# Optimization experiments

Measured on AMD Instinct MI355X. Metric: run time of the kernel, lower is better.

The kernel has to match this reference:

```python
import jax, jax.numpy as jnp
import numpy as np

D = 256      # model_dim
H = 8        # num_heads
S = 256      # tokens per channel
CH = [4, 2, 6, 4]  # multiplex_channels_per_sample


def _make_padding(ch, s):
    # Build gather indices / mask mapping packed tokens [T] -> padded [B, Lmax]
    B = len(ch)
    lens = [c * s for c in ch]
    T = sum(lens)
    Lmax = max(lens)
    pad_idx = np.zeros((B, Lmax), dtype=np.int32)
    pad_mask = np.zeros((B, Lmax), dtype=bool)
    off = 0
    for b, L in enumerate(lens):
        pad_idx[b, :L] = np.arange(off, off + L, dtype=np.int32)
        pad_mask[b, :L] = True
        off += L
    return jnp.asarray(pad_idx), jnp.asarray(pad_mask)


def setup_inputs() -> dict:
    key = jax.random.key(0)
    ks = jax.random.split(key, 16)
    C = sum(CH)
    x_query = jax.random.normal(ks[0], (C, S, D), jnp.float32)
    x_keyval = jax.random.normal(ks[1], (C, S, D), jnp.float32)
    pos = jax.random.normal(ks[2], (C, S, D), jnp.float32)
    pad_idx, pad_mask = _make_padding(CH, S)
    sc = 1.0 / np.sqrt(D)
    Wq = jax.random.normal(ks[3], (D, D), jnp.float32) * sc
    Wk = jax.random.normal(ks[4], (D, D), jnp.float32) * sc
    Wv = jax.random.normal(ks[5], (D, D), jnp.float32) * sc
    Wo = jax.random.normal(ks[6], (D, D), jnp.float32) * sc
    bq = jax.random.normal(ks[7], (D,), jnp.float32) * 0.02
    bk = jax.random.normal(ks[8], (D,), jnp.float32) * 0.02
    bv = jax.random.normal(ks[9], (D,), jnp.float32) * 0.02
    bo = jax.random.normal(ks[10], (D,), jnp.float32) * 0.02
    return {"x_query": x_query, "x_keyval": x_keyval, "pos": pos,
            "pad_idx": pad_idx, "pad_mask": pad_mask,
            "Wq": Wq, "bq": bq, "Wk": Wk, "bk": bk,
            "Wv": Wv, "bv": bv, "Wo": Wo, "bo": bo}


def reference(x_query, x_keyval, pos, pad_idx, pad_mask,
              Wq, bq, Wk, bk, Wv, bv, Wo, bo):
    C, s, d = x_query.shape
    T = C * s
    dh = d // H
    # MHA with positional embedding: pos is added to query and key inputs
    # (query_pos = key_pos = pos in the original forward), value is raw.
    q_in = (x_query + pos).reshape(T, d)
    k_in = (x_keyval + pos).reshape(T, d)
    v_in = x_keyval.reshape(T, d)
    q = q_in @ Wq + bq
    k = k_in @ Wk + bk
    v = v_in @ Wv + bv
    # Pad packed ragged tokens into [B, Lmax, D] per cu_seq_len segments
    B, Lmax = pad_idx.shape
    qp = q[pad_idx].reshape(B, Lmax, H, dh)
    kp = k[pad_idx].reshape(B, Lmax, H, dh)
    vp = v[pad_idx].reshape(B, Lmax, H, dh)
    scores = jnp.einsum('bqhd,bkhd->bhqk', qp, kp) / jnp.sqrt(jnp.asarray(dh, q.dtype))
    neg = jnp.asarray(jnp.finfo(scores.dtype).min, scores.dtype)
    scores = jnp.where(pad_mask[:, None, None, :], scores, neg)
    attn = jax.nn.softmax(scores, axis=-1)
    out = jnp.einsum('bhqk,bkhd->bqhd', attn, vp).reshape(B, Lmax, d)
    out = out * pad_mask[..., None]
    # Scatter padded outputs back to packed layout [T, D]
    flat = jnp.zeros((T, d), out.dtype).at[pad_idx.reshape(-1)].add(out.reshape(-1, d))
    flat = flat @ Wo + bo
    return flat.reshape(C, s, d)
```

## Files before the change

kernel.cpp:

```cpp
#include <hip/hip_runtime.h>
#include <math.h>

#define Dm 256
#define Tt 4096

typedef short  s16x8 __attribute__((ext_vector_type(8)));
typedef float  f32x4 __attribute__((ext_vector_type(4)));

__device__ __forceinline__ ushort f2bf(float x) {
    union { float f; unsigned u; } v; v.f = x;
    unsigned r = v.u + 0x7fffu + ((v.u >> 16) & 1u);
    return (ushort)(r >> 16);
}

__device__ __forceinline__ int ppos(int row, int key) {
    return row * 64 + (key & 7) + ((((key >> 3) ^ (row >> 1)) & 7) << 3);
}

__global__ __launch_bounds__(256)
void convert_x(const float* __restrict__ xq, const float* __restrict__ xkv,
               const float* __restrict__ pos,
               ushort* __restrict__ A0, ushort* __restrict__ A1, ushort* __restrict__ A2)
{
    const int t = threadIdx.x;
    const int m = blockIdx.y;
    const float* xin = (m == 0) ? xq : xkv;
    ushort* out = (m == 0) ? A0 : (m == 1) ? A1 : A2;
    const int token = blockIdx.x * 32 + (t >> 3);
    const int c0 = (t & 7) * 32;
    const float* p = &xin[token * Dm + c0];
    const float* pp = &pos[token * Dm + c0];
    #pragma unroll
    for (int i = 0; i < 4; ++i) {
        float4 fa = *(const float4*)&p[i * 8];
        float4 fb = *(const float4*)&p[i * 8 + 4];
        if (m < 2) {
            float4 pa = *(const float4*)&pp[i * 8], pb = *(const float4*)&pp[i * 8 + 4];
            fa.x += pa.x; fa.y += pa.y; fa.z += pa.z; fa.w += pa.w;
            fb.x += pb.x; fb.y += pb.y; fb.z += pb.z; fb.w += pb.w;
        }
        s16x8 v8;
        v8[0] = (short)f2bf(fa.x); v8[1] = (short)f2bf(fa.y);
        v8[2] = (short)f2bf(fa.z); v8[3] = (short)f2bf(fa.w);
        v8[4] = (short)f2bf(fb.x); v8[5] = (short)f2bf(fb.y);
        v8[6] = (short)f2bf(fb.z); v8[7] = (short)f2bf(fb.w);
        *(s16x8*)&out[token * Dm + c0 + i * 8] = v8;
    }
}

__global__ __launch_bounds__(256)
void prep_w(const float* __restrict__ Wq, const float* __restrict__ Wk,
            const float* __restrict__ Wv, const float* __restrict__ Wo,
            ushort* __restrict__ Wt)
{
    __shared__ float T[64][65];
    const int tid = threadIdx.x;
    const int m = blockIdx.y;
    const int i = blockIdx.x >> 2, j = blockIdx.x & 3;
    const float* W = (m == 0) ? Wq : (m == 1) ? Wk : (m == 2) ? Wv : Wo;

    #pragma unroll
    for (int s = 0; s < 4; ++s) {
        int idx = s * 256 + tid;
        int r = idx >> 4, c4 = (idx & 15) << 2;
        float4 f = *(const float4*)&W[(i * 64 + r) * Dm + j * 64 + c4];
        T[c4 + 0][r] = f.x; T[c4 + 1][r] = f.y;
        T[c4 + 2][r] = f.z; T[c4 + 3][r] = f.w;
    }
    __syncthreads();
    #pragma unroll
    for (int s = 0; s < 2; ++s) {
        int idx = s * 256 + tid;
        int cr = idx >> 3, k8 = (idx & 7) << 3;
        s16x8 v8;
        #pragma unroll
        for (int jj = 0; jj < 8; ++jj) v8[jj] = (short)f2bf(T[cr][k8 + jj]);
        *(s16x8*)&Wt[m * 65536 + (j * 64 + cr) * Dm + i * 64 + k8] = v8;
    }
}

__global__ __launch_bounds__(256)
void proj_gemm(const ushort* __restrict__ A0, const ushort* __restrict__ A1,
               const ushort* __restrict__ A2, const ushort* __restrict__ Wt,
               const float* __restrict__ bq, const float* __restrict__ bk,
               const float* __restrict__ bv,
               ushort* __restrict__ qo, ushort* __restrict__ ko, ushort* __restrict__ vo)
{
    __shared__ __align__(16) ushort A_s[64 * 64];
    __shared__ __align__(16) ushort B_s[64 * 64];
    const int tid = threadIdx.x;
    const int lane = tid & 63, g = lane >> 4, myrow = lane & 15, w = tid >> 6;
    const int t0 = blockIdx.x * 64;
    const int c0 = blockIdx.y * 64;
    const int m  = blockIdx.z;
    const ushort* Ab = (m == 0) ? A0 : (m == 1) ? A1 : A2;
    const ushort* WT = Wt + m * 65536;
    const float* bias = (m == 0) ? bq : (m == 1) ? bk : bv;
    ushort* out = (m == 0) ? qo : (m == 1) ? ko : vo;

    f32x4 acc[4] = {};
    for (int ks = 0; ks < 4; ++ks) {
        const int k0 = ks * 64;
        #pragma unroll
        for (int s = 0; s < 2; ++s) {
            int idx = s * 256 + tid;
            int r = idx >> 3, c = idx & 7;
            *(s16x8*)&A_s[r * 64 + ((c ^ (r & 7)) << 3)] =
                *(const s16x8*)&Ab[(t0 + r) * Dm + k0 + c * 8];
            *(s16x8*)&B_s[r * 64 + ((c ^ (r & 7)) << 3)] =
                *(const s16x8*)&WT[(c0 + r) * Dm + k0 + c * 8];
        }
        __syncthreads();
        const int arow = w * 16 + myrow;
        #pragma unroll
        for (int kk = 0; kk < 2; ++kk) {
            s16x8 a = *(s16x8*)&A_s[arow * 64 + (((g + 4 * kk) ^ (arow & 7)) << 3)];
            #pragma unroll
            for (int ct = 0; ct < 4; ++ct) {
                int brow = ct * 16 + myrow;
                s16x8 b = *(s16x8*)&B_s[brow * 64 + (((g + 4 * kk) ^ (brow & 7)) << 3)];
                acc[ct] = __builtin_amdgcn_mfma_f32_16x16x32_bf16(a, b, acc[ct], 0, 0, 0);
            }
        }
        __syncthreads();
    }
    const float qsc = 0.17677669529663687f;
    #pragma unroll
    for (int ct = 0; ct < 4; ++ct) {
        int col = c0 + ct * 16 + myrow;
        float bval = bias[col];
        #pragma unroll
        for (int r = 0; r < 4; ++r) {
            int tok = t0 + w * 16 + 4 * g + r;
            float vv = acc[ct][r] + bval;
            if (m == 0) vv *= qsc;
            out[tok * Dm + col] = f2bf(vv);
        }
    }
}

__global__ __launch_bounds__(256)
void transp_v(const ushort* __restrict__ v, ushort* __restrict__ vT)
{
    __shared__ __align__(16) ushort T_s[64 * 72];
    const int tid = threadIdx.x;
    const int t0 = blockIdx.x * 64;
    const int c0 = blockIdx.y * 64;
    #pragma unroll
    for (int s = 0; s < 2; ++s) {
        int idx = s * 256 + tid;
        int row = idx >> 3, c8 = (idx & 7) << 3;
        s16x8 d = *(const s16x8*)&v[(t0 + row) * Dm + c0 + c8];
        #pragma unroll
        for (int j = 0; j < 8; ++j) {
            int c = c8 + j;
            T_s[c * 72 + (row ^ ((c & 7) << 3))] = (ushort)d[j];
        }
    }
    __syncthreads();
    #pragma unroll
    for (int s = 0; s < 2; ++s) {
        int idx = s * 256 + tid;
        int c = idx >> 3, k8 = (idx & 7) << 3;
        s16x8 d = *(const s16x8*)&T_s[c * 72 + (k8 ^ ((c & 7) << 3))];
        *(s16x8*)&vT[(c0 + c) * Tt + t0 + k8] = d;
    }
}

__global__ __launch_bounds__(256)
void attn3(const ushort* __restrict__ q, const ushort* __restrict__ kb,
           const ushort* __restrict__ vT, ushort* __restrict__ o)
{
    __shared__ __align__(16) ushort P_s[4][16 * 64];
    __shared__ float cmb[96 * 36];
    const int tid = threadIdx.x;
    const int lane = tid & 63, g = lane >> 4, myrow = lane & 15, w = tid >> 6;
    const int h = blockIdx.x & 7, qt = blockIdx.x >> 3;

    int off, L;
    if (qt < 32)      { off = 0;    L = 1024; }
    else if (qt < 48) { off = 1024; L = 512;  }
    else if (qt < 96) { off = 1536; L = 1536; }
    else              { off = 3072; L = 1024; }
    const int qrow0 = qt * 32;
    const int Lw = L >> 2;
    const int kbeg = off + w * Lw;
    const int ntk = Lw >> 6;

    s16x8 qf[2];
    qf[0] = *(const s16x8*)&q[(qrow0 + myrow) * Dm + h * 32 + g * 8];
    qf[1] = *(const s16x8*)&q[(qrow0 + 16 + myrow) * Dm + h * 32 + g * 8];

    f32x4 aO[2][2] = {};
    float mr[2][4], lr[2][4];
    #pragma unroll
    for (int s = 0; s < 2; ++s)
        #pragma unroll
        for (int r = 0; r < 4; ++r) { mr[s][r] = -INFINITY; lr[s][r] = 0.f; }

    for (int t = 0; t < ntk; ++t) {
        const int kt0 = kbeg + t * 64;
        s16x8 kf[4];
        #pragma unroll
        for (int kt = 0; kt < 4; ++kt)
            kf[kt] = *(const s16x8*)&kb[(kt0 + kt * 16 + myrow) * Dm + h * 32 + g * 8];
        s16x8 vfa[2], vfb[2];
        #pragma unroll
        for (int kk = 0; kk < 2; ++kk) {
            vfa[kk] = *(const s16x8*)&vT[(h * 32 + myrow) * Tt + kt0 + kk * 32 + g * 8];
            vfb[kk] = *(const s16x8*)&vT[(h * 32 + 16 + myrow) * Tt + kt0 + kk * 32 + g * 8];
        }

        #pragma unroll
        for (int s = 0; s < 2; ++s) {
            const f32x4 zero = {};
            f32x4 s4[4];
            #pragma unroll
            for (int kt = 0; kt < 4; ++kt)
                s4[kt] = __builtin_amdgcn_mfma_f32_16x16x32_bf16(qf[s], kf[kt], zero, 0, 0, 0);

            float mt[4], sc[4], ps[4];
            #pragma unroll
            for (int r = 0; r < 4; ++r) {
                float a = fmaxf(fmaxf(s4[0][r], s4[1][r]), fmaxf(s4[2][r], s4[3][r]));
                a = fmaxf(a, __shfl_xor(a, 1));
                a = fmaxf(a, __shfl_xor(a, 2));
                a = fmaxf(a, __shfl_xor(a, 4));
                a = fmaxf(a, __shfl_xor(a, 8));
                mt[r] = a;
            }
            #pragma unroll
            for (int r = 0; r < 4; ++r) {
                float mn = fmaxf(mr[s][r], mt[r]);
                sc[r] = __expf(mr[s][r] - mn);
                mr[s][r] = mn;
                ps[r] = 0.f;
            }
            asm volatile("s_waitcnt lgkmcnt(0)" ::: "memory");
            __builtin_amdgcn_sched_barrier(0);
            #pragma unroll
            for (int kt = 0; kt < 4; ++kt) {
                #pragma unroll
                for (int r = 0; r < 4; ++r) {
                    float p = __expf(s4[kt][r] - mr[s][r]);
                    ps[r] += p;
                    P_s[w][ppos(4 * g + r, 16 * kt + myrow)] = f2bf(p);
                }
            }
            #pragma unroll
            for (int r = 0; r < 4; ++r) {
                float sps = ps[r];
                sps += __shfl_xor(sps, 1);
                sps += __shfl_xor(sps, 2);
                sps += __shfl_xor(sps, 4);
                sps += __shfl_xor(sps, 8);
                lr[s][r] = lr[s][r] * sc[r] + sps;
                aO[s][0][r] *= sc[r];
                aO[s][1][r] *= sc[r];
            }
            asm volatile("s_waitcnt lgkmcnt(0)" ::: "memory");
            __builtin_amdgcn_sched_barrier(0);
            #pragma unroll
            for (int kk = 0; kk < 2; ++kk) {
                s16x8 ap = *(const s16x8*)&P_s[w][ppos(myrow, (g + 4 * kk) * 8)];
                aO[s][0] = __builtin_amdgcn_mfma_f32_16x16x32_bf16(ap, vfa[kk], aO[s][0], 0, 0, 0);
                aO[s][1] = __builtin_amdgcn_mfma_f32_16x16x32_bf16(ap, vfb[kk], aO[s][1], 0, 0, 0);
            }
        }
    }

    __syncthreads();
    if (w > 0) {
        #pragma unroll
        for (int s = 0; s < 2; ++s)
            #pragma unroll
            for (int r = 0; r < 4; ++r) {
                int row = (w - 1) * 32 + s * 16 + 4 * g + r;
                cmb[row * 36 + myrow]      = aO[s][0][r];
                cmb[row * 36 + 16 + myrow] = aO[s][1][r];
                if (myrow == 0) { cmb[row * 36 + 32] = mr[s][r]; cmb[row * 36 + 33] = lr[s][r]; }
            }
    }
    __syncthreads();
    if (w == 0) {
        #pragma unroll
        for (int s = 0; s < 2; ++s) {
            #pragma unroll
            for (int r = 0; r < 4; ++r) {
                #pragma unroll
                for (int ww = 0; ww < 3; ++ww) {
                    int row = ww * 32 + s * 16 + 4 * g + r;
                    float m2 = cmb[row * 36 + 32], l2 = cmb[row * 36 + 33];
                    float mn = fmaxf(mr[s][r], m2);
                    float a1 = __expf(mr[s][r] - mn), a2 = __expf(m2 - mn);
                    mr[s][r] = mn;
                    lr[s][r] = lr[s][r] * a1 + l2 * a2;
                    aO[s][0][r] = aO[s][0][r] * a1 + cmb[row * 36 + myrow] * a2;
                    aO[s][1][r] = aO[s][1][r] * a1 + cmb[row * 36 + 16 + myrow] * a2;
                }
                float inv = 1.0f / lr[s][r];
                int orow = (qrow0 + s * 16 + 4 * g + r) * Dm + h * 32;
                o[orow + myrow]      = f2bf(aO[s][0][r] * inv);
                o[orow + 16 + myrow] = f2bf(aO[s][1][r] * inv);
            }
        }
    }
}

__global__ __launch_bounds__(256)
void oproj_mfma(const ushort* __restrict__ A, const ushort* __restrict__ Wt3,
                const float* __restrict__ bo, float* __restrict__ out)
{
    __shared__ __align__(16) ushort A_s[32 * 64];
    __shared__ __align__(16) ushort B_s[64 * 64];
    const int tid = threadIdx.x;
    const int lane = tid & 63, g = lane >> 4, myrow = lane & 15, w = tid >> 6;
    const int sh = w >> 1, ch = w & 1;
    const int t0 = blockIdx.x * 32;
    const int c0 = blockIdx.y * 64;

    f32x4 acc[2] = {};
    for (int ks = 0; ks < 4; ++ks) {
        const int k0 = ks * 64;
        {
            int r = tid >> 3, c = tid & 7;
            *(s16x8*)&A_s[r * 64 + ((c ^ (r & 7)) << 3)] =
                *(const s16x8*)&A[(t0 + r) * Dm + k0 + c * 8];
        }
        #pragma unroll
        for (int s = 0; s < 2; ++s) {
            int idx = s * 256 + tid;
            int r = idx >> 3, c = idx & 7;
            *(s16x8*)&B_s[r * 64 + ((c ^ (r & 7)) << 3)] =
                *(const s16x8*)&Wt3[(c0 + r) * Dm + k0 + c * 8];
        }
        __syncthreads();
        const int arow = sh * 16 + myrow;
        #pragma unroll
        for (int kk = 0; kk < 2; ++kk) {
            s16x8 a = *(s16x8*)&A_s[arow * 64 + (((g + 4 * kk) ^ (arow & 7)) << 3)];
            #pragma unroll
            for (int ct = 0; ct < 2; ++ct) {
                int brow = ch * 32 + ct * 16 + myrow;
                s16x8 b = *(s16x8*)&B_s[brow * 64 + (((g + 4 * kk) ^ (brow & 7)) << 3)];
                acc[ct] = __builtin_amdgcn_mfma_f32_16x16x32_bf16(a, b, acc[ct], 0, 0, 0);
            }
        }
        __syncthreads();
    }
    #pragma unroll
    for (int ct = 0; ct < 2; ++ct) {
        int col = c0 + ch * 32 + ct * 16 + myrow;
        float bval = bo[col];
        #pragma unroll
        for (int r = 0; r < 4; ++r)
            out[(t0 + sh * 16 + 4 * g + r) * Dm + col] = acc[ct][r] + bval;
    }
}

extern "C" void kernel_launch(void* const* d_in, const int* in_sizes, int n_in,
                              void* d_out, int out_size, void* d_ws, size_t ws_size,
                              hipStream_t stream) {
    const float* xq  = (const float*)d_in[0];
    const float* xkv = (const float*)d_in[1];
    const float* pos = (const float*)d_in[2];
    const float* Wq  = (const float*)d_in[5];
    const float* bq  = (const float*)d_in[6];
    const float* Wk  = (const float*)d_in[7];
    const float* bk  = (const float*)d_in[8];
    const float* Wv  = (const float*)d_in[9];
    const float* bv  = (const float*)d_in[10];
    const float* Wo  = (const float*)d_in[11];
    const float* bo  = (const float*)d_in[12];

    ushort* Abf = (ushort*)d_ws;
    ushort* qb  = Abf + 3 * Tt * Dm;
    ushort* kbp = qb + Tt * Dm;
    ushort* vb  = kbp + Tt * Dm;
    ushort* vTt = vb + Tt * Dm;
    ushort* ab  = vTt + Tt * Dm;
    ushort* Wt  = ab + Tt * Dm;

    convert_x<<<dim3(Tt / 32, 3), 256, 0, stream>>>(xq, xkv, pos, Abf,
                                                    Abf + Tt * Dm, Abf + 2 * Tt * Dm);
    prep_w<<<dim3(16, 4), 256, 0, stream>>>(Wq, Wk, Wv, Wo, Wt);
    proj_gemm<<<dim3(64, 4, 3), 256, 0, stream>>>(Abf, Abf + Tt * Dm, Abf + 2 * Tt * Dm,
                                                  Wt, bq, bk, bv, qb, kbp, vb);
    transp_v<<<dim3(64, 4), 256, 0, stream>>>(vb, vTt);
    attn3<<<dim3(1024), 256, 0, stream>>>(qb, kbp, vTt, ab);
    oproj_mfma<<<dim3(128, 4), 256, 0, stream>>>(ab, Wt + 3 * 65536, bo, (float*)d_out);
}
```

Before: 135.1 us.

## Load GEMM operands straight to registers, enlarge row tiles, drop attention LDS waits

The projection and output GEMMs no longer stage A and W tiles through shared memory. Each wave now loads MFMA operands directly from global memory and computes a 128-row by 64-column tile, which halves the projection grid and shrinks the output-projection grid by a factor of four. This removes LDS traffic and block barriers, but relies on L1/L2 to serve the W rows shared across waves and lowers the block count. Separately, the attention kernel drops two explicit lgkmcnt waits and scheduling barriers around the P_s shared-memory writes and reads, leaving ordering to the compiler.

Result: slower. 151.8 us (+12.3%).

```diff
diff --git a/kernel.cpp b/kernel.cpp
--- a/kernel.cpp
+++ b/kernel.cpp
@@ -86,11 +86,9 @@
                const float* __restrict__ bv,
                ushort* __restrict__ qo, ushort* __restrict__ ko, ushort* __restrict__ vo)
 {
-    __shared__ __align__(16) ushort A_s[64 * 64];
-    __shared__ __align__(16) ushort B_s[64 * 64];
     const int tid = threadIdx.x;
     const int lane = tid & 63, g = lane >> 4, myrow = lane & 15, w = tid >> 6;
-    const int t0 = blockIdx.x * 64;
+    const int t0 = blockIdx.x * 128;
     const int c0 = blockIdx.y * 64;
     const int m  = blockIdx.z;
     const ushort* Ab = (m == 0) ? A0 : (m == 1) ? A1 : A2;
@@ -98,31 +96,21 @@
     const float* bias = (m == 0) ? bq : (m == 1) ? bk : bv;
     ushort* out = (m == 0) ? qo : (m == 1) ? ko : vo;
 
-    f32x4 acc[4] = {};
-    for (int ks = 0; ks < 4; ++ks) {
-        const int k0 = ks * 64;
-        #pragma unroll
-        for (int s = 0; s < 2; ++s) {
-            int idx = s * 256 + tid;
-            int r = idx >> 3, c = idx & 7;
-            *(s16x8*)&A_s[r * 64 + ((c ^ (r & 7)) << 3)] =
-                *(const s16x8*)&Ab[(t0 + r) * Dm + k0 + c * 8];
-            *(s16x8*)&B_s[r * 64 + ((c ^ (r & 7)) << 3)] =
-                *(const s16x8*)&WT[(c0 + r) * Dm + k0 + c * 8];
-        }
-        __syncthreads();
-        const int arow = w * 16 + myrow;
-        #pragma unroll
-        for (int kk = 0; kk < 2; ++kk) {
-            s16x8 a = *(s16x8*)&A_s[arow * 64 + (((g + 4 * kk) ^ (arow & 7)) << 3)];
-            #pragma unroll
-            for (int ct = 0; ct < 4; ++ct) {
-                int brow = ct * 16 + myrow;
-                s16x8 b = *(s16x8*)&B_s[brow * 64 + (((g + 4 * kk) ^ (brow & 7)) << 3)];
-                acc[ct] = __builtin_amdgcn_mfma_f32_16x16x32_bf16(a, b, acc[ct], 0, 0, 0);
-            }
-        }
-        __syncthreads();
+    const int rowA0 = t0 + w * 16 + myrow;
+    const int rowA1 = rowA0 + 64;
+
+    f32x4 acc[2][4] = {};
+    #pragma unroll 2
+    for (int kk = 0; kk < 8; ++kk) {
+        const int kofs = kk * 32 + g * 8;
+        s16x8 a0 = *(const s16x8*)&Ab[rowA0 * Dm + kofs];
+        s16x8 a1 = *(const s16x8*)&Ab[rowA1 * Dm + kofs];
+        #pragma unroll
+        for (int ct = 0; ct < 4; ++ct) {
+            s16x8 b = *(const s16x8*)&WT[(c0 + ct * 16 + myrow) * Dm + kofs];
+            acc[0][ct] = __builtin_amdgcn_mfma_f32_16x16x32_bf16(a0, b, acc[0][ct], 0, 0, 0);
+            acc[1][ct] = __builtin_amdgcn_mfma_f32_16x16x32_bf16(a1, b, acc[1][ct], 0, 0, 0);
+        }
     }
     const float qsc = 0.17677669529663687f;
     #pragma unroll
@@ -130,11 +118,14 @@
         int col = c0 + ct * 16 + myrow;
         float bval = bias[col];
         #pragma unroll
-        for (int r = 0; r < 4; ++r) {
-            int tok = t0 + w * 16 + 4 * g + r;
-            float vv = acc[ct][r] + bval;
-            if (m == 0) vv *= qsc;
-            out[tok * Dm + col] = f2bf(vv);
+        for (int st = 0; st < 2; ++st) {
+            #pragma unroll
+            for (int r = 0; r < 4; ++r) {
+                int tok = t0 + st * 64 + w * 16 + 4 * g + r;
+                float vv = acc[st][ct][r] + bval;
+                if (m == 0) vv *= qsc;
+                out[tok * Dm + col] = f2bf(vv);
+            }
         }
     }
 }
@@ -168,7 +159,7 @@
 }
 
 __global__ __launch_bounds__(256)
-void attn3(const ushort* __restrict__ q, const ushort* __restrict__ kb,
+void attn4(const ushort* __restrict__ q, const ushort* __restrict__ kb,
            const ushort* __restrict__ vT, ushort* __restrict__ o)
 {
     __shared__ __align__(16) ushort P_s[4][16 * 64];
@@ -236,8 +227,6 @@
                 mr[s][r] = mn;
                 ps[r] = 0.f;
             }
-            asm volatile("s_waitcnt lgkmcnt(0)" ::: "memory");
-            __builtin_amdgcn_sched_barrier(0);
             #pragma unroll
             for (int kt = 0; kt < 4; ++kt) {
                 #pragma unroll
@@ -258,8 +247,6 @@
                 aO[s][0][r] *= sc[r];
                 aO[s][1][r] *= sc[r];
             }
-            asm volatile("s_waitcnt lgkmcnt(0)" ::: "memory");
-            __builtin_amdgcn_sched_barrier(0);
             #pragma unroll
             for (int kk = 0; kk < 2; ++kk) {
                 s16x8 ap = *(const s16x8*)&P_s[w][ppos(myrow, (g + 4 * kk) * 8)];
@@ -311,50 +298,37 @@
 void oproj_mfma(const ushort* __restrict__ A, const ushort* __restrict__ Wt3,
                 const float* __restrict__ bo, float* __restrict__ out)
 {
-    __shared__ __align__(16) ushort A_s[32 * 64];
-    __shared__ __align__(16) ushort B_s[64 * 64];
     const int tid = threadIdx.x;
     const int lane = tid & 63, g = lane >> 4, myrow = lane & 15, w = tid >> 6;
-    const int sh = w >> 1, ch = w & 1;
-    const int t0 = blockIdx.x * 32;
+    const int t0 = blockIdx.x * 128;
     const int c0 = blockIdx.y * 64;
 
-    f32x4 acc[2] = {};
-    for (int ks = 0; ks < 4; ++ks) {
-        const int k0 = ks * 64;
-        {
-            int r = tid >> 3, c = tid & 7;
-            *(s16x8*)&A_s[r * 64 + ((c ^ (r & 7)) << 3)] =
-                *(const s16x8*)&A[(t0 + r) * Dm + k0 + c * 8];
-        }
-        #pragma unroll
-        for (int s = 0; s < 2; ++s) {
-            int idx = s * 256 + tid;
-            int r = idx >> 3, c = idx & 7;
-            *(s16x8*)&B_s[r * 64 + ((c ^ (r & 7)) << 3)] =
-                *(const s16x8*)&Wt3[(c0 + r) * Dm + k0 + c * 8];
-        }
-        __syncthreads();
-        const int arow = sh * 16 + myrow;
-        #pragma unroll
-        for (int kk = 0; kk < 2; ++kk) {
-            s16x8 a = *(s16x8*)&A_s[arow * 64 + (((g + 4 * kk) ^ (arow & 7)) << 3)];
-            #pragma unroll
-            for (int ct = 0; ct < 2; ++ct) {
-                int brow = ch * 32 + ct * 16 + myrow;
-                s16x8 b = *(s16x8*)&B_s[brow * 64 + (((g + 4 * kk) ^ (brow & 7)) << 3)];
-                acc[ct] = __builtin_amdgcn_mfma_f32_16x16x32_bf16(a, b, acc[ct], 0, 0, 0);
-            }
-        }
-        __syncthreads();
-    }
-    #pragma unroll
-    for (int ct = 0; ct < 2; ++ct) {
-        int col = c0 + ch * 32 + ct * 16 + myrow;
+    const int rowA0 = t0 + w * 16 + myrow;
+    const int rowA1 = rowA0 + 64;
+
+    f32x4 acc[2][4] = {};
+    #pragma unroll 2
+    for (int kk = 0; kk < 8; ++kk) {
+        const int kofs = kk * 32 + g * 8;
+        s16x8 a0 = *(const s16x8*)&A[rowA0 * Dm + kofs];
+        s16x8 a1 = *(const s16x8*)&A[rowA1 * Dm + kofs];
+        #pragma unroll
+        for (int ct = 0; ct < 4; ++ct) {
+            s16x8 b = *(const s16x8*)&Wt3[(c0 + ct * 16 + myrow) * Dm + kofs];
+            acc[0][ct] = __builtin_amdgcn_mfma_f32_16x16x32_bf16(a0, b, acc[0][ct], 0, 0, 0);
+            acc[1][ct] = __builtin_amdgcn_mfma_f32_16x16x32_bf16(a1, b, acc[1][ct], 0, 0, 0);
+        }
+    }
+    #pragma unroll
+    for (int ct = 0; ct < 4; ++ct) {
+        int col = c0 + ct * 16 + myrow;
         float bval = bo[col];
         #pragma unroll
-        for (int r = 0; r < 4; ++r)
-            out[(t0 + sh * 16 + 4 * g + r) * Dm + col] = acc[ct][r] + bval;
+        for (int st = 0; st < 2; ++st) {
+            #pragma unroll
+            for (int r = 0; r < 4; ++r)
+                out[(t0 + st * 64 + w * 16 + 4 * g + r) * Dm + col] = acc[st][ct][r] + bval;
+        }
     }
 }
 
@@ -384,9 +358,9 @@
     convert_x<<<dim3(Tt / 32, 3), 256, 0, stream>>>(xq, xkv, pos, Abf,
                                                     Abf + Tt * Dm, Abf + 2 * Tt * Dm);
     prep_w<<<dim3(16, 4), 256, 0, stream>>>(Wq, Wk, Wv, Wo, Wt);
-    proj_gemm<<<dim3(64, 4, 3), 256, 0, stream>>>(Abf, Abf + Tt * Dm, Abf + 2 * Tt * Dm,
+    proj_gemm<<<dim3(32, 4, 3), 256, 0, stream>>>(Abf, Abf + Tt * Dm, Abf + 2 * Tt * Dm,
                                                   Wt, bq, bk, bv, qb, kbp, vb);
     transp_v<<<dim3(64, 4), 256, 0, stream>>>(vb, vTt);
-    attn3<<<dim3(1024), 256, 0, stream>>>(qb, kbp, vTt, ab);
-    oproj_mfma<<<dim3(128, 4), 256, 0, stream>>>(ab, Wt + 3 * 65536, bo, (float*)d_out);
-}
+    attn4<<<dim3(1024), 256, 0, stream>>>(qb, kbp, vTt, ab);
+    oproj_mfma<<<dim3(32, 4), 256, 0, stream>>>(ab, Wt + 3 * 65536, bo, (float*)d_out);
+}
```

## Compute transposed scores so softmax P stays in registers via shuffles

Applied to the files above, without the earlier changes.

The attention kernel now computes S^T = K·Q^T, so each lane holds one query column and the row max and sum need only two cross-lane shuffles instead of four per row. The probability tile is packed to bf16 and redistributed with __shfl into the MFMA B-operand layout, which removes the LDS round trip and its waitcnt barriers. The Q scale now folds in log2(e) so exp2f replaces __expf. The epilogue writes vectorized float4 and ushort4 values. The cost is sixteen extra shuffles and selects per PV step.

After: 131.5 us. 1.03x faster.

```diff
diff --git a/kernel.cpp b/kernel.cpp
--- a/kernel.cpp
+++ b/kernel.cpp
@@ -11,10 +11,6 @@
     union { float f; unsigned u; } v; v.f = x;
     unsigned r = v.u + 0x7fffu + ((v.u >> 16) & 1u);
     return (ushort)(r >> 16);
-}
-
-__device__ __forceinline__ int ppos(int row, int key) {
-    return row * 64 + (key & 7) + ((((key >> 3) ^ (row >> 1)) & 7) << 3);
 }
 
 __global__ __launch_bounds__(256)
@@ -124,7 +120,7 @@
         }
         __syncthreads();
     }
-    const float qsc = 0.17677669529663687f;
+    const float qsc = 0.25503482f;
     #pragma unroll
     for (int ct = 0; ct < 4; ++ct) {
         int col = c0 + ct * 16 + myrow;
@@ -168,11 +164,10 @@
 }
 
 __global__ __launch_bounds__(256)
-void attn3(const ushort* __restrict__ q, const ushort* __restrict__ kb,
+void attn5(const ushort* __restrict__ q, const ushort* __restrict__ kb,
            const ushort* __restrict__ vT, ushort* __restrict__ o)
 {
-    __shared__ __align__(16) ushort P_s[4][16 * 64];
-    __shared__ float cmb[96 * 36];
+    __shared__ __align__(16) float cmb[96 * 36];
     const int tid = threadIdx.x;
     const int lane = tid & 63, g = lane >> 4, myrow = lane & 15, w = tid >> 6;
     const int h = blockIdx.x & 7, qt = blockIdx.x >> 3;
@@ -191,12 +186,9 @@
     qf[0] = *(const s16x8*)&q[(qrow0 + myrow) * Dm + h * 32 + g * 8];
     qf[1] = *(const s16x8*)&q[(qrow0 + 16 + myrow) * Dm + h * 32 + g * 8];
 
-    f32x4 aO[2][2] = {};
-    float mr[2][4], lr[2][4];
-    #pragma unroll
-    for (int s = 0; s < 2; ++s)
-        #pragma unroll
-        for (int r = 0; r < 4; ++r) { mr[s][r] = -INFINITY; lr[s][r] = 0.f; }
+    f32x4 aT[2][2] = {};
+    float mr[2] = {-INFINITY, -INFINITY};
+    float lr[2] = {0.f, 0.f};
 
     for (int t = 0; t < ntk; ++t) {
         const int kt0 = kbeg + t * 64;
@@ -214,57 +206,64 @@
         #pragma unroll
         for (int s = 0; s < 2; ++s) {
             const f32x4 zero = {};
-            f32x4 s4[4];
+            f32x4 sc4[4];
             #pragma unroll
             for (int kt = 0; kt < 4; ++kt)
-                s4[kt] = __builtin_amdgcn_mfma_f32_16x16x32_bf16(qf[s], kf[kt], zero, 0, 0, 0);
-
-            float mt[4], sc[4], ps[4];
-            #pragma unroll
-            for (int r = 0; r < 4; ++r) {
-                float a = fmaxf(fmaxf(s4[0][r], s4[1][r]), fmaxf(s4[2][r], s4[3][r]));
-                a = fmaxf(a, __shfl_xor(a, 1));
-                a = fmaxf(a, __shfl_xor(a, 2));
-                a = fmaxf(a, __shfl_xor(a, 4));
-                a = fmaxf(a, __shfl_xor(a, 8));
-                mt[r] = a;
-            }
-            #pragma unroll
-            for (int r = 0; r < 4; ++r) {
-                float mn = fmaxf(mr[s][r], mt[r]);
-                sc[r] = __expf(mr[s][r] - mn);
-                mr[s][r] = mn;
-                ps[r] = 0.f;
-            }
-            asm volatile("s_waitcnt lgkmcnt(0)" ::: "memory");
-            __builtin_amdgcn_sched_barrier(0);
-            #pragma unroll
-            for (int kt = 0; kt < 4; ++kt) {
+                sc4[kt] = __builtin_amdgcn_mfma_f32_16x16x32_bf16(kf[kt], qf[s], zero, 0, 0, 0);
+
+            float mx0 = fmaxf(fmaxf(sc4[0][0], sc4[0][1]), fmaxf(sc4[0][2], sc4[0][3]));
+            float mx1 = fmaxf(fmaxf(sc4[1][0], sc4[1][1]), fmaxf(sc4[1][2], sc4[1][3]));
+            float mx2 = fmaxf(fmaxf(sc4[2][0], sc4[2][1]), fmaxf(sc4[2][2], sc4[2][3]));
+            float mx3 = fmaxf(fmaxf(sc4[3][0], sc4[3][1]), fmaxf(sc4[3][2], sc4[3][3]));
+            float mx = fmaxf(fmaxf(mx0, mx1), fmaxf(mx2, mx3));
+            mx = fmaxf(mx, __shfl_xor(mx, 16));
+            mx = fmaxf(mx, __shfl_xor(mx, 32));
+            float mn = fmaxf(mr[s], mx);
+            float scl = exp2f(mr[s] - mn);
+            mr[s] = mn;
+
+            float p[4][4];
+            float psum = 0.f;
+            #pragma unroll
+            for (int kt = 0; kt < 4; ++kt)
                 #pragma unroll
                 for (int r = 0; r < 4; ++r) {
-                    float p = __expf(s4[kt][r] - mr[s][r]);
-                    ps[r] += p;
-                    P_s[w][ppos(4 * g + r, 16 * kt + myrow)] = f2bf(p);
+                    p[kt][r] = exp2f(sc4[kt][r] - mn);
+                    psum += p[kt][r];
                 }
-            }
-            #pragma unroll
-            for (int r = 0; r < 4; ++r) {
-                float sps = ps[r];
-                sps += __shfl_xor(sps, 1);
-                sps += __shfl_xor(sps, 2);
-                sps += __shfl_xor(sps, 4);
-                sps += __shfl_xor(sps, 8);
-                lr[s][r] = lr[s][r] * sc[r] + sps;
-                aO[s][0][r] *= sc[r];
-                aO[s][1][r] *= sc[r];
-            }
-            asm volatile("s_waitcnt lgkmcnt(0)" ::: "memory");
-            __builtin_amdgcn_sched_barrier(0);
+            psum += __shfl_xor(psum, 16);
+            psum += __shfl_xor(psum, 32);
+            lr[s] = lr[s] * scl + psum;
+            #pragma unroll
+            for (int r = 0; r < 4; ++r) { aT[s][0][r] *= scl; aT[s][1][r] *= scl; }
+
+            unsigned pk[4][2];
+            #pragma unroll
+            for (int kt = 0; kt < 4; ++kt) {
+                pk[kt][0] = (unsigned)f2bf(p[kt][0]) | ((unsigned)f2bf(p[kt][1]) << 16);
+                pk[kt][1] = (unsigned)f2bf(p[kt][2]) | ((unsigned)f2bf(p[kt][3]) << 16);
+            }
+
+            const int lA = (g & 1) * 32 + myrow;
+            const int lB = lA + 16;
+            const bool hi = (g >> 1) != 0;
             #pragma unroll
             for (int kk = 0; kk < 2; ++kk) {
-                s16x8 ap = *(const s16x8*)&P_s[w][ppos(myrow, (g + 4 * kk) * 8)];
-                aO[s][0] = __builtin_amdgcn_mfma_f32_16x16x32_bf16(ap, vfa[kk], aO[s][0], 0, 0, 0);
-                aO[s][1] = __builtin_amdgcn_mfma_f32_16x16x32_bf16(ap, vfb[kk], aO[s][1], 0, 0, 0);
+                int a0 = __shfl((int)pk[2 * kk][0],     lA, 64);
+                int a1 = __shfl((int)pk[2 * kk][1],     lA, 64);
+                int a2 = __shfl((int)pk[2 * kk][0],     lB, 64);
+                int a3 = __shfl((int)pk[2 * kk][1],     lB, 64);
+                int b0 = __shfl((int)pk[2 * kk + 1][0], lA, 64);
+                int b1 = __shfl((int)pk[2 * kk + 1][1], lA, 64);
+                int b2 = __shfl((int)pk[2 * kk + 1][0], lB, 64);
+                int b3 = __shfl((int)pk[2 * kk + 1][1], lB, 64);
+                union { int i[4]; s16x8 v; } pb;
+                pb.i[0] = hi ? b0 : a0;
+                pb.i[1] = hi ? b1 : a1;
+                pb.i[2] = hi ? b2 : a2;
+                pb.i[3] = hi ? b3 : a3;
+                aT[s][0] = __builtin_amdgcn_mfma_f32_16x16x32_bf16(vfa[kk], pb.v, aT[s][0], 0, 0, 0);
+                aT[s][1] = __builtin_amdgcn_mfma_f32_16x16x32_bf16(vfb[kk], pb.v, aT[s][1], 0, 0, 0);
             }
         }
     }
@@ -272,36 +271,46 @@
     __syncthreads();
     if (w > 0) {
         #pragma unroll
-        for (int s = 0; s < 2; ++s)
-            #pragma unroll
-            for (int r = 0; r < 4; ++r) {
-                int row = (w - 1) * 32 + s * 16 + 4 * g + r;
-                cmb[row * 36 + myrow]      = aO[s][0][r];
-                cmb[row * 36 + 16 + myrow] = aO[s][1][r];
-                if (myrow == 0) { cmb[row * 36 + 32] = mr[s][r]; cmb[row * 36 + 33] = lr[s][r]; }
-            }
+        for (int s = 0; s < 2; ++s) {
+            int row = (w - 1) * 32 + 16 * s + myrow;
+            *(float4*)&cmb[row * 36 + 4 * g]      = (float4){aT[s][0][0], aT[s][0][1], aT[s][0][2], aT[s][0][3]};
+            *(float4*)&cmb[row * 36 + 16 + 4 * g] = (float4){aT[s][1][0], aT[s][1][1], aT[s][1][2], aT[s][1][3]};
+            if (g == 0) { cmb[row * 36 + 32] = mr[s]; cmb[row * 36 + 33] = lr[s]; }
+        }
     }
     __syncthreads();
     if (w == 0) {
         #pragma unroll
         for (int s = 0; s < 2; ++s) {
             #pragma unroll
-            for (int r = 0; r < 4; ++r) {
-                #pragma unroll
-                for (int ww = 0; ww < 3; ++ww) {
-                    int row = ww * 32 + s * 16 + 4 * g + r;
-                    float m2 = cmb[row * 36 + 32], l2 = cmb[row * 36 + 33];
-                    float mn = fmaxf(mr[s][r], m2);
-                    float a1 = __expf(mr[s][r] - mn), a2 = __expf(m2 - mn);
-                    mr[s][r] = mn;
-                    lr[s][r] = lr[s][r] * a1 + l2 * a2;
-                    aO[s][0][r] = aO[s][0][r] * a1 + cmb[row * 36 + myrow] * a2;
-                    aO[s][1][r] = aO[s][1][r] * a1 + cmb[row * 36 + 16 + myrow] * a2;
-                }
-                float inv = 1.0f / lr[s][r];
-                int orow = (qrow0 + s * 16 + 4 * g + r) * Dm + h * 32;
-                o[orow + myrow]      = f2bf(aO[s][0][r] * inv);
-                o[orow + 16 + myrow] = f2bf(aO[s][1][r] * inv);
+            for (int ww = 0; ww < 3; ++ww) {
+                int row = ww * 32 + 16 * s + myrow;
+                float m2 = cmb[row * 36 + 32], l2 = cmb[row * 36 + 33];
+                float mn = fmaxf(mr[s], m2);
+                float a1 = exp2f(mr[s] - mn), a2 = exp2f(m2 - mn);
+                mr[s] = mn;
+                lr[s] = lr[s] * a1 + l2 * a2;
+                float4 c0_ = *(float4*)&cmb[row * 36 + 4 * g];
+                float4 c1_ = *(float4*)&cmb[row * 36 + 16 + 4 * g];
+                aT[s][0][0] = aT[s][0][0] * a1 + c0_.x * a2;
+                aT[s][0][1] = aT[s][0][1] * a1 + c0_.y * a2;
+                aT[s][0][2] = aT[s][0][2] * a1 + c0_.z * a2;
+                aT[s][0][3] = aT[s][0][3] * a1 + c0_.w * a2;
+                aT[s][1][0] = aT[s][1][0] * a1 + c1_.x * a2;
+                aT[s][1][1] = aT[s][1][1] * a1 + c1_.y * a2;
+                aT[s][1][2] = aT[s][1][2] * a1 + c1_.z * a2;
+                aT[s][1][3] = aT[s][1][3] * a1 + c1_.w * a2;
+            }
+            float inv = 1.0f / lr[s];
+            int base = (qrow0 + 16 * s + myrow) * Dm + h * 32;
+            #pragma unroll
+            for (int half = 0; half < 2; ++half) {
+                ushort4 r4;
+                r4.x = f2bf(aT[s][half][0] * inv);
+                r4.y = f2bf(aT[s][half][1] * inv);
+                r4.z = f2bf(aT[s][half][2] * inv);
+                r4.w = f2bf(aT[s][half][3] * inv);
+                *(ushort4*)&o[base + 16 * half + 4 * g] = r4;
             }
         }
     }
@@ -387,6 +396,6 @@
     proj_gemm<<<dim3(64, 4, 3), 256, 0, stream>>>(Abf, Abf + Tt * Dm, Abf + 2 * Tt * Dm,
                                                   Wt, bq, bk, bv, qb, kbp, vb);
     transp_v<<<dim3(64, 4), 256, 0, stream>>>(vb, vTt);
-    attn3<<<dim3(1024), 256, 0, stream>>>(qb, kbp, vTt, ab);
+    attn5<<<dim3(1024), 256, 0, stream>>>(qb, kbp, vTt, ab);
     oproj_mfma<<<dim3(128, 4), 256, 0, stream>>>(ab, Wt + 3 * 65536, bo, (float*)d_out);
 }
```
